# Optimization experiments

Hardware: AMD Instinct MI355X
Metric: run time of the kernel (lower is better)

The kernel has to match this reference:

```python
import jax, jax.numpy as jnp
import numpy as np

# ---- static forest structure: 1024 complete binary trees of depth 9 ----
N_TREES = 1024
DEPTH = 9
NPT = 2 ** (DEPTH + 1) - 1            # 1023 nodes per tree
DIM = N_TREES * NPT                    # 1,047,552 total nodes
C = 10                                 # hidden states
M = 128                                # emission alphabet
N_GEN = 4                              # parallel generative models
LEVEL_SIZES = [N_TREES * 2 ** (k + 1) for k in range(DEPTH)]
LEVEL_START = np.concatenate([[0], np.cumsum(LEVEL_SIZES)]).astype(np.int64)
TREE_OFF = np.arange(N_TREES, dtype=np.int64) * NPT


def _build_forest():
    parents, children = [], []
    for k in range(DEPTH):
        ch = np.arange(2 ** (k + 1) - 1, 2 ** (k + 2) - 1, dtype=np.int64)  # depth k+1 nodes
        pa = (ch - 1) // 2                                                   # their parents (depth k)
        children.append((TREE_OFF[:, None] + ch[None, :]).ravel())
        parents.append((TREE_OFF[:, None] + pa[None, :]).ravel())
    leaves = (TREE_OFF[:, None] + np.arange(NPT // 2, NPT, dtype=np.int64)[None, :]).ravel()
    trees_ind = np.repeat(np.arange(N_TREES, dtype=np.int64), NPT)
    return np.concatenate(parents), np.concatenate(children), leaves, trees_ind


def setup_inputs() -> dict:
    key = jax.random.key(0)
    k1, k2, k3, k4 = jax.random.split(key, 4)
    parents, children, leaves, trees_ind = _build_forest()
    return {
        "x": jax.random.randint(k4, (DIM,), 0, M, dtype=jnp.int32),
        "A": jax.random.normal(k1, (C, C, N_GEN), jnp.float32) * 2.5,
        "B": jax.random.normal(k2, (C, M, N_GEN), jnp.float32) * 2.5,
        "Pi": jax.random.normal(k3, (C, N_GEN), jnp.float32) * 2.5,
        "parents": jnp.asarray(parents, jnp.int32),
        "children": jnp.asarray(children, jnp.int32),
        "trees_ind": jnp.asarray(trees_ind, jnp.int32),
        "leaves": jnp.asarray(leaves, jnp.int32),
    }


def _upward(x, A, B, Pi, parents, children, trees_ind, leaves):
    # softmax reparameterization (vectorized over the n_gen axis)
    smA = jax.nn.softmax(A, axis=0)    # P(parent state i | child state j), cols sum over i
    smB = jax.nn.softmax(B, axis=1)    # emission distribution per state
    smPi = jax.nn.softmax(Pi, axis=0)  # leaf prior

    beta = jnp.zeros((DIM, C, N_GEN), smA.dtype)
    t_beta = jnp.zeros((DIM, C, N_GEN), smA.dtype)
    ll = jnp.zeros((DIM, N_GEN), smA.dtype)

    # leaves: beta = Pi * B[:, x_leaf], normalized
    B_leaf = jnp.swapaxes(smB[:, x[leaves]], 0, 1)            # [L, C, G]
    b = smPi[None, :, :] * B_leaf
    nu = b.sum(axis=1)                                         # [L, G]
    beta = beta.at[leaves].set(b / nu[:, None, :])
    ll = ll.at[leaves].set(jnp.log(nu))

    # bottom-up sweep over levels (static loop over tree depth)
    for k in reversed(range(DEPTH)):
        s, e = int(LEVEL_START[k]), int(LEVEL_START[k + 1])
        pa, ch = parents[s:e], children[s:e]
        beta_ch = beta[ch]                                     # [E, C, G]
        tb_ch = jnp.einsum('ijg,ejg->eig', smA, beta_ch)       # sum over child state j
        sums = jax.ops.segment_sum(tb_ch, pa, num_segments=DIM)
        cnt = jax.ops.segment_sum(jnp.ones((e - s,), smA.dtype), pa, num_segments=DIM)
        t_beta = t_beta + sums / jnp.maximum(cnt, 1.0)[:, None, None]  # scatter-mean over children
        # unique parents at this level = all depth-k nodes (static for complete trees)
        u = jnp.asarray((TREE_OFF[:, None] + np.arange(2 ** k - 1, 2 ** (k + 1) - 1)[None, :]).ravel(), jnp.int32)
        B_u = jnp.swapaxes(smB[:, x[u]], 0, 1)                 # [U, C, G]
        bl = t_beta[u] * B_u
        nu = bl.sum(axis=1)
        beta = beta.at[u].set(bl / nu[:, None, :])
        ll = ll.at[u].set(jnp.log(nu))

    # per-tree log-likelihood: scatter-sum node terms over trees_ind
    return jax.ops.segment_sum(ll, trees_ind, num_segments=N_TREES)  # [n_trees, G]


def reference(x, A, B, Pi, parents, children, trees_ind, leaves):
    return _upward(x, A, B, Pi, parents, children, trees_ind, leaves)
```

## Files before the change

kernel.cpp:

```cpp
#include <hip/hip_runtime.h>
#include <math.h>

#define NC     10
#define NCP    12
#define NM     128
#define NGEN   4
#define NPT    1023
#define NTREES 1024

#define RCPF(x) __builtin_amdgcn_rcpf(x)
#define WAVE_FENCE() __builtin_amdgcn_wave_barrier()

struct F12 { float4 a, b, c; };

__device__ __forceinline__ F12 ld12(const float* p) {
    F12 r; const float4* q = (const float4*)p;
    r.a = q[0]; r.b = q[1]; r.c = q[2]; return r;
}
__device__ __forceinline__ void unpack10(float* t, const F12& r) {
    t[0] = r.a.x; t[1] = r.a.y; t[2] = r.a.z; t[3] = r.a.w;
    t[4] = r.b.x; t[5] = r.b.y; t[6] = r.b.z; t[7] = r.b.w;
    t[8] = r.c.x; t[9] = r.c.y;
}
__device__ __forceinline__ void fma10(float* t, const F12& c, float s) {
    t[0] += c.a.x * s; t[1] += c.a.y * s; t[2] += c.a.z * s; t[3] += c.a.w * s;
    t[4] += c.b.x * s; t[5] += c.b.y * s; t[6] += c.b.z * s; t[7] += c.b.w * s;
    t[8] += c.c.x * s; t[9] += c.c.y * s;
}
__device__ __forceinline__ void mul10(float* t, const F12& r) {
    t[0] *= r.a.x; t[1] *= r.a.y; t[2] *= r.a.z; t[3] *= r.a.w;
    t[4] *= r.b.x; t[5] *= r.b.y; t[6] *= r.b.z; t[7] *= r.b.w;
    t[8] *= r.c.x; t[9] *= r.c.y;
}
__device__ __forceinline__ float sum10(const float* v) {
    return (((v[0] + v[1]) + (v[2] + v[3])) + ((v[4] + v[5]) + (v[6] + v[7]))) + (v[8] + v[9]);
}

__device__ __forceinline__ float half_subtree(const F12* acol,
                                              const float (*sBT)[NCP],
                                              const float (*sBTpi)[NCP],
                                              int xl0, int xl1, int xl2, int xl3,
                                              int x8a, int x8b, int x7, float* b7out)
{
    float b0[NC], b1[NC], sc[NC], t8a[NC], t8b[NC];

    unpack10(b0, ld12(&sBTpi[xl0][0]));
    unpack10(b1, ld12(&sBTpi[xl1][0]));
    float nu0 = sum10(b0), nu1 = sum10(b1);
    #pragma unroll
    for (int j = 0; j < NC; ++j) sc[j] = b0[j] * nu1 + b1[j] * nu0;
    #pragma unroll
    for (int i = 0; i < NC; ++i) t8a[i] = 0.f;
    #pragma unroll
    for (int j = 0; j < NC; ++j) fma10(t8a, acol[j], sc[j]);
    mul10(t8a, ld12(&sBT[x8a][0]));
    const float nu8a = sum10(t8a);

    unpack10(b0, ld12(&sBTpi[xl2][0]));
    unpack10(b1, ld12(&sBTpi[xl3][0]));
    nu0 = sum10(b0); nu1 = sum10(b1);
    #pragma unroll
    for (int j = 0; j < NC; ++j) sc[j] = b0[j] * nu1 + b1[j] * nu0;
    #pragma unroll
    for (int i = 0; i < NC; ++i) t8b[i] = 0.f;
    #pragma unroll
    for (int j = 0; j < NC; ++j) fma10(t8b, acol[j], sc[j]);
    mul10(t8b, ld12(&sBT[x8b][0]));
    const float nu8b = sum10(t8b);

    #pragma unroll
    for (int j = 0; j < NC; ++j) sc[j] = t8a[j] * nu8b + t8b[j] * nu8a;
    float t7[NC];
    #pragma unroll
    for (int i = 0; i < NC; ++i) t7[i] = 0.f;
    #pragma unroll
    for (int j = 0; j < NC; ++j) fma10(t7, acol[j], sc[j]);
    mul10(t7, ld12(&sBT[x7][0]));
    const float nu7 = sum10(t7);
    const float r = RCPF(nu7);
    #pragma unroll
    for (int j = 0; j < NC; ++j) b7out[j] = t7[j] * r;
    return __logf(nu7);
}

__device__ __forceinline__ float fused_step_ip(const F12* acol, const float (*sBT)[NCP],
                                               float* buf, int l,
                                               int xc0, int xc1, int xp)
{
    float t0[NC], t1[NC];
    #pragma unroll
    for (int i = 0; i < NC; ++i) { t0[i] = 0.f; t1[i] = 0.f; }
    #pragma unroll
    for (int j = 0; j < NC; ++j) {
        float4 gv = *(const float4*)(buf + j * 64 + 4 * l);
        fma10(t0, acol[j], gv.x + gv.y);
        fma10(t1, acol[j], gv.z + gv.w);
    }
    mul10(t0, ld12(&sBT[xc0][0]));
    mul10(t1, ld12(&sBT[xc1][0]));
    const float nu0 = sum10(t0), nu1 = sum10(t1);
    float tp[NC];
    #pragma unroll
    for (int i = 0; i < NC; ++i) tp[i] = 0.f;
    #pragma unroll
    for (int j = 0; j < NC; ++j) fma10(tp, acol[j], t0[j] * nu1 + t1[j] * nu0);
    mul10(tp, ld12(&sBT[xp][0]));
    const float nup = sum10(tp);
    const float rp = RCPF(nup);
    #pragma unroll
    for (int j = 0; j < NC; ++j) buf[j * 64 + l] = tp[j] * rp;
    return __logf(nup);
}

__global__ __launch_bounds__(256)
void htmm_fused(const int* __restrict__ x,
                const float* __restrict__ A,
                const float* __restrict__ B,
                const float* __restrict__ Pi,
                float* __restrict__ out)
{
    __shared__ __align__(16) float sACol[NC][NCP];
    __shared__ __align__(16) float sBT[NM][NCP];
    __shared__ __align__(16) float sBTpi[NM][NCP];
    __shared__ __align__(16) float sB6[4][NC][64];

    const int bid = blockIdx.x;
    const int g = bid >> 8;
    const int treeBase = (bid & 255) * 4;
    const int tid = threadIdx.x;
    const int u = tid >> 6, lane = tid & 63;

    const int tree = treeBase + u;
    const int tb = tree * NPT;

    int xl[8];
    #pragma unroll
    for (int k = 0; k < 8; ++k) xl[k] = x[tb + 511 + 8 * lane + k];
    int x8v[4];
    #pragma unroll
    for (int c = 0; c < 4; ++c) x8v[c] = x[tb + 255 + 4 * lane + c];
    const int x7a = x[tb + 127 + 2 * lane];
    const int x7b = x[tb + 128 + 2 * lane];
    const int x6v = x[tb + 63 + lane];

    float piv[NC];
    {
        float mx = -1e30f;
        #pragma unroll
        for (int i = 0; i < NC; ++i) { piv[i] = Pi[i * NGEN + g]; mx = fmaxf(mx, piv[i]); }
        float sm = 0.f;
        #pragma unroll
        for (int i = 0; i < NC; ++i) { piv[i] = __expf(piv[i] - mx); sm += piv[i]; }
        const float rs = 1.f / sm;
        #pragma unroll
        for (int i = 0; i < NC; ++i) piv[i] *= rs;
    }

    for (int c = u; c < NC; c += 4) {
        float e0 = __expf(B[(c * NM + lane) * NGEN + g]);
        float e1 = __expf(B[(c * NM + lane + 64) * NGEN + g]);
        float sm = e0 + e1;
        #pragma unroll
        for (int off = 32; off; off >>= 1) sm += __shfl_xor(sm, off);
        const float rs = 1.f / sm;
        const float v0 = e0 * rs, v1 = e1 * rs;
        sBT[lane][c]        = v0;
        sBT[lane + 64][c]   = v1;
        sBTpi[lane][c]      = piv[c] * v0;
        sBTpi[lane + 64][c] = piv[c] * v1;
    }
    if (tid >= 128 && tid < 128 + NC) {
        const int j = tid - 128;
        float col[NC], mx = -1e30f;
        #pragma unroll
        for (int i = 0; i < NC; ++i) { col[i] = A[(i * NC + j) * NGEN + g]; mx = fmaxf(mx, col[i]); }
        float sm = 0.f;
        #pragma unroll
        for (int i = 0; i < NC; ++i) { col[i] = __expf(col[i] - mx); sm += col[i]; }
        const float rs = 0.5f / sm;
        #pragma unroll
        for (int i = 0; i < NC; ++i) sACol[j][i] = col[i] * rs;
    }
    __syncthreads();

    F12 acol[NC];
    #pragma unroll
    for (int j = 0; j < NC; ++j) acol[j] = ld12(&sACol[j][0]);

    float b7a[NC], b7b[NC];
    float llacc;
    llacc  = half_subtree(acol, sBT, sBTpi, xl[0], xl[1], xl[2], xl[3],
                          x8v[0], x8v[1], x7a, b7a);
    llacc += half_subtree(acol, sBT, sBTpi, xl[4], xl[5], xl[6], xl[7],
                          x8v[2], x8v[3], x7b, b7b);

    {
        float sc[NC], t6[NC];
        #pragma unroll
        for (int j = 0; j < NC; ++j) sc[j] = b7a[j] + b7b[j];
        #pragma unroll
        for (int i = 0; i < NC; ++i) t6[i] = 0.f;
        #pragma unroll
        for (int j = 0; j < NC; ++j) fma10(t6, acol[j], sc[j]);
        mul10(t6, ld12(&sBT[x6v][0]));
        const float nup = sum10(t6);
        llacc += __logf(nup);
        const float rp = RCPF(nup);
        #pragma unroll
        for (int j = 0; j < NC; ++j) sB6[u][j][lane] = t6[j] * rp;
    }

    WAVE_FENCE();
    float lla = 0.f;
    if (lane < 16)
        lla = fused_step_ip(acol, sBT, &sB6[u][0][0], lane,
                            x[tb + 31 + 2 * lane], x[tb + 32 + 2 * lane],
                            x[tb + 15 + lane]);
    llacc += lla;
    WAVE_FENCE();
    float llb = 0.f;
    if (lane < 4)
        llb = fused_step_ip(acol, sBT, &sB6[u][0][0], lane,
                            x[tb + 7 + 2 * lane], x[tb + 8 + 2 * lane],
                            x[tb + 3 + lane]);
    llacc += llb;
    WAVE_FENCE();
    if (lane == 0)
        llacc += fused_step_ip(acol, sBT, &sB6[u][0][0], 0,
                               x[tb + 1], x[tb + 2], x[tb + 0]);

    #pragma unroll
    for (int off = 32; off; off >>= 1) llacc += __shfl_down(llacc, off);
    if (lane == 0) out[tree * NGEN + g] = llacc;
}

extern "C" void kernel_launch(void* const* d_in, const int* in_sizes, int n_in,
                              void* d_out, int out_size, void* d_ws, size_t ws_size,
                              hipStream_t stream) {
    const int*   x  = (const int*)d_in[0];
    const float* A  = (const float*)d_in[1];
    const float* B  = (const float*)d_in[2];
    const float* Pi = (const float*)d_in[3];
    float* out = (float*)d_out;
    htmm_fused<<<NTREES, 256, 0, stream>>>(x, A, B, Pi, out);
}
```

Measured before the change: 26.68 us.

## Split softmax setup into prologue kernel and run main pass one wave per block

Moves the per-generator softmax of A, B and Pi into a small setup kernel that writes padded tables to workspace. The main kernel then launches 4096 single-wave blocks that copy the emission table into LDS with vector loads, with no block-wide barrier. Pi is applied in registers instead of keeping a second LDS table, which halves LDS use and should allow more blocks per CU. The cost is a second kernel launch and a dependency between the two kernels. The fallback fused path gains a dead dummy call to the subtree helper.

```diff
diff --git a/kernel.cpp b/kernel.cpp
--- a/kernel.cpp
+++ b/kernel.cpp
@@ -8,6 +8,11 @@
 #define NPT    1023
 #define NTREES 1024
 
+#define WS_AC(g)   ((g) * (NC * NCP))
+#define WS_PI(g)   (4 * NC * NCP + (g) * NCP)
+#define WS_BT(g)   (4 * NC * NCP + 4 * NCP + (g) * (NM * NCP))
+#define WS_FLOATS  (4 * NC * NCP + 4 * NCP + 4 * NM * NCP)
+
 #define RCPF(x) __builtin_amdgcn_rcpf(x)
 #define WAVE_FENCE() __builtin_amdgcn_wave_barrier()
 
@@ -38,14 +43,16 @@
 
 __device__ __forceinline__ float half_subtree(const F12* acol,
                                               const float (*sBT)[NCP],
-                                              const float (*sBTpi)[NCP],
+                                              const float* piv,
                                               int xl0, int xl1, int xl2, int xl3,
                                               int x8a, int x8b, int x7, float* b7out)
 {
     float b0[NC], b1[NC], sc[NC], t8a[NC], t8b[NC];
 
-    unpack10(b0, ld12(&sBTpi[xl0][0]));
-    unpack10(b1, ld12(&sBTpi[xl1][0]));
+    unpack10(b0, ld12(&sBT[xl0][0]));
+    unpack10(b1, ld12(&sBT[xl1][0]));
+    #pragma unroll
+    for (int j = 0; j < NC; ++j) { b0[j] *= piv[j]; b1[j] *= piv[j]; }
     float nu0 = sum10(b0), nu1 = sum10(b1);
     #pragma unroll
     for (int j = 0; j < NC; ++j) sc[j] = b0[j] * nu1 + b1[j] * nu0;
@@ -56,8 +63,10 @@
     mul10(t8a, ld12(&sBT[x8a][0]));
     const float nu8a = sum10(t8a);
 
-    unpack10(b0, ld12(&sBTpi[xl2][0]));
-    unpack10(b1, ld12(&sBTpi[xl3][0]));
+    unpack10(b0, ld12(&sBT[xl2][0]));
+    unpack10(b1, ld12(&sBT[xl3][0]));
+    #pragma unroll
+    for (int j = 0; j < NC; ++j) { b0[j] *= piv[j]; b1[j] *= piv[j]; }
     nu0 = sum10(b0); nu1 = sum10(b1);
     #pragma unroll
     for (int j = 0; j < NC; ++j) sc[j] = b0[j] * nu1 + b1[j] * nu0;
@@ -110,6 +119,147 @@
     #pragma unroll
     for (int j = 0; j < NC; ++j) buf[j * 64 + l] = tp[j] * rp;
     return __logf(nup);
+}
+
+__global__ __launch_bounds__(128)
+void htmm_setup(const float* __restrict__ A,
+                const float* __restrict__ B,
+                const float* __restrict__ Pi,
+                float* __restrict__ ws)
+{
+    const int g = blockIdx.x;
+    const int tid = threadIdx.x;
+    const int wave = tid >> 6, lane = tid & 63;
+    float* bt = ws + WS_BT(g);
+
+    for (int c = wave; c < NC; c += 2) {
+        float e0 = __expf(B[(c * NM + lane) * NGEN + g]);
+        float e1 = __expf(B[(c * NM + lane + 64) * NGEN + g]);
+        float s = e0 + e1;
+        #pragma unroll
+        for (int off = 32; off; off >>= 1) s += __shfl_xor(s, off);
+        const float rs = 1.f / s;
+        bt[lane * NCP + c]        = e0 * rs;
+        bt[(lane + 64) * NCP + c] = e1 * rs;
+    }
+    if (tid < NM) { bt[tid * NCP + 10] = 0.f; bt[tid * NCP + 11] = 0.f; }
+
+    if (tid < NC) {
+        const int j = tid;
+        float col[NC], mx = -1e30f;
+        #pragma unroll
+        for (int i = 0; i < NC; ++i) { col[i] = A[(i * NC + j) * NGEN + g]; mx = fmaxf(mx, col[i]); }
+        float s = 0.f;
+        #pragma unroll
+        for (int i = 0; i < NC; ++i) { col[i] = __expf(col[i] - mx); s += col[i]; }
+        const float rs = 0.5f / s;
+        float* ac = ws + WS_AC(g) + j * NCP;
+        #pragma unroll
+        for (int i = 0; i < NC; ++i) ac[i] = col[i] * rs;
+        ac[10] = 0.f; ac[11] = 0.f;
+    }
+    if (tid == 32) {
+        float col[NC], mx = -1e30f;
+        #pragma unroll
+        for (int i = 0; i < NC; ++i) { col[i] = Pi[i * NGEN + g]; mx = fmaxf(mx, col[i]); }
+        float s = 0.f;
+        #pragma unroll
+        for (int i = 0; i < NC; ++i) { col[i] = __expf(col[i] - mx); s += col[i]; }
+        const float rs = 1.f / s;
+        float* pp = ws + WS_PI(g);
+        #pragma unroll
+        for (int i = 0; i < NC; ++i) pp[i] = col[i] * rs;
+        pp[10] = 0.f; pp[11] = 0.f;
+    }
+}
+
+__global__ __launch_bounds__(64)
+void htmm_main(const int* __restrict__ x,
+               const float* __restrict__ ws,
+               float* __restrict__ out)
+{
+    __shared__ __align__(16) float sBT[NM][NCP];
+    __shared__ __align__(16) float sB6[NC][64];
+
+    const int bid  = blockIdx.x;
+    const int tree = bid >> 2;
+    const int g    = bid & 3;
+    const int lane = threadIdx.x;
+    const int tb   = tree * NPT;
+
+    const float4* src = (const float4*)(ws + WS_BT(g));
+    float4 cp0 = src[0 * 64 + lane], cp1 = src[1 * 64 + lane];
+    float4 cp2 = src[2 * 64 + lane], cp3 = src[3 * 64 + lane];
+    float4 cp4 = src[4 * 64 + lane], cp5 = src[5 * 64 + lane];
+
+    int xl[8];
+    #pragma unroll
+    for (int k = 0; k < 8; ++k) xl[k] = x[tb + 511 + 8 * lane + k];
+    int x8v[4];
+    #pragma unroll
+    for (int c = 0; c < 4; ++c) x8v[c] = x[tb + 255 + 4 * lane + c];
+    const int x7a = x[tb + 127 + 2 * lane];
+    const int x7b = x[tb + 128 + 2 * lane];
+    const int x6v = x[tb + 63 + lane];
+
+    F12 acol[NC];
+    #pragma unroll
+    for (int j = 0; j < NC; ++j) acol[j] = ld12(ws + WS_AC(g) + j * NCP);
+    float piv[NC];
+    { F12 pv = ld12(ws + WS_PI(g)); unpack10(piv, pv); }
+
+    {
+        float4* dst = (float4*)&sBT[0][0];
+        dst[0 * 64 + lane] = cp0; dst[1 * 64 + lane] = cp1;
+        dst[2 * 64 + lane] = cp2; dst[3 * 64 + lane] = cp3;
+        dst[4 * 64 + lane] = cp4; dst[5 * 64 + lane] = cp5;
+    }
+    WAVE_FENCE();
+
+    float b7a[NC], b7b[NC];
+    float llacc;
+    llacc  = half_subtree(acol, sBT, piv, xl[0], xl[1], xl[2], xl[3],
+                          x8v[0], x8v[1], x7a, b7a);
+    llacc += half_subtree(acol, sBT, piv, xl[4], xl[5], xl[6], xl[7],
+                          x8v[2], x8v[3], x7b, b7b);
+    {
+        float sc[NC], t6[NC];
+        #pragma unroll
+        for (int j = 0; j < NC; ++j) sc[j] = b7a[j] + b7b[j];
+        #pragma unroll
+        for (int i = 0; i < NC; ++i) t6[i] = 0.f;
+        #pragma unroll
+        for (int j = 0; j < NC; ++j) fma10(t6, acol[j], sc[j]);
+        mul10(t6, ld12(&sBT[x6v][0]));
+        const float nup = sum10(t6);
+        llacc += __logf(nup);
+        const float rp = RCPF(nup);
+        #pragma unroll
+        for (int j = 0; j < NC; ++j) sB6[j][lane] = t6[j] * rp;
+    }
+
+    WAVE_FENCE();
+    float lla = 0.f;
+    if (lane < 16)
+        lla = fused_step_ip(acol, sBT, &sB6[0][0], lane,
+                            x[tb + 31 + 2 * lane], x[tb + 32 + 2 * lane],
+                            x[tb + 15 + lane]);
+    llacc += lla;
+    WAVE_FENCE();
+    float llb = 0.f;
+    if (lane < 4)
+        llb = fused_step_ip(acol, sBT, &sB6[0][0], lane,
+                            x[tb + 7 + 2 * lane], x[tb + 8 + 2 * lane],
+                            x[tb + 3 + lane]);
+    llacc += llb;
+    WAVE_FENCE();
+    if (lane == 0)
+        llacc += fused_step_ip(acol, sBT, &sB6[0][0], 0,
+                               x[tb + 1], x[tb + 2], x[tb + 0]);
+
+    #pragma unroll
+    for (int off = 32; off; off >>= 1) llacc += __shfl_down(llacc, off);
+    if (lane == 0) out[tree * NGEN + g] = llacc;
 }
 
 __global__ __launch_bounds__(256)
@@ -129,7 +279,6 @@
     const int treeBase = (bid & 255) * 4;
     const int tid = threadIdx.x;
     const int u = tid >> 6, lane = tid & 63;
-
     const int tree = treeBase + u;
     const int tb = tree * NPT;
 
@@ -155,7 +304,6 @@
         #pragma unroll
         for (int i = 0; i < NC; ++i) piv[i] *= rs;
     }
-
     for (int c = u; c < NC; c += 4) {
         float e0 = __expf(B[(c * NM + lane) * NGEN + g]);
         float e1 = __expf(B[(c * NM + lane + 64) * NGEN + g]);
@@ -187,13 +335,59 @@
     #pragma unroll
     for (int j = 0; j < NC; ++j) acol[j] = ld12(&sACol[j][0]);
 
+    float ones[NC];
+    #pragma unroll
+    for (int i = 0; i < NC; ++i) ones[i] = 1.f;
+
     float b7a[NC], b7b[NC];
     float llacc;
-    llacc  = half_subtree(acol, sBT, sBTpi, xl[0], xl[1], xl[2], xl[3],
-                          x8v[0], x8v[1], x7a, b7a);
-    llacc += half_subtree(acol, sBT, sBTpi, xl[4], xl[5], xl[6], xl[7],
-                          x8v[2], x8v[3], x7b, b7b);
-
+    llacc  = half_subtree(acol, sBT, ones, 0, 0, 0, 0, 0, 0, 0, b7a);
+    llacc = 0.f;
+    {
+        float b0[NC], b1[NC], sc[NC], t8a[NC], t8b[NC];
+        #pragma unroll
+        for (int h = 0; h < 2; ++h) {
+            const int* xh = xl + 4 * h;
+            const int x8a = x8v[2 * h], x8b = x8v[2 * h + 1];
+            const int x7 = h ? x7b : x7a;
+            unpack10(b0, ld12(&sBTpi[xh[0]][0]));
+            unpack10(b1, ld12(&sBTpi[xh[1]][0]));
+            float nu0 = sum10(b0), nu1 = sum10(b1);
+            #pragma unroll
+            for (int j = 0; j < NC; ++j) sc[j] = b0[j] * nu1 + b1[j] * nu0;
+            #pragma unroll
+            for (int i = 0; i < NC; ++i) t8a[i] = 0.f;
+            #pragma unroll
+            for (int j = 0; j < NC; ++j) fma10(t8a, acol[j], sc[j]);
+            mul10(t8a, ld12(&sBT[x8a][0]));
+            const float nu8a = sum10(t8a);
+            unpack10(b0, ld12(&sBTpi[xh[2]][0]));
+            unpack10(b1, ld12(&sBTpi[xh[3]][0]));
+            nu0 = sum10(b0); nu1 = sum10(b1);
+            #pragma unroll
+            for (int j = 0; j < NC; ++j) sc[j] = b0[j] * nu1 + b1[j] * nu0;
+            #pragma unroll
+            for (int i = 0; i < NC; ++i) t8b[i] = 0.f;
+            #pragma unroll
+            for (int j = 0; j < NC; ++j) fma10(t8b, acol[j], sc[j]);
+            mul10(t8b, ld12(&sBT[x8b][0]));
+            const float nu8b = sum10(t8b);
+            #pragma unroll
+            for (int j = 0; j < NC; ++j) sc[j] = t8a[j] * nu8b + t8b[j] * nu8a;
+            float t7[NC];
+            #pragma unroll
+            for (int i = 0; i < NC; ++i) t7[i] = 0.f;
+            #pragma unroll
+            for (int j = 0; j < NC; ++j) fma10(t7, acol[j], sc[j]);
+            mul10(t7, ld12(&sBT[x7][0]));
+            const float nu7 = sum10(t7);
+            const float r = RCPF(nu7);
+            float* dst = h ? b7b : b7a;
+            #pragma unroll
+            for (int j = 0; j < NC; ++j) dst[j] = t7[j] * r;
+            llacc += __logf(nu7);
+        }
+    }
     {
         float sc[NC], t6[NC];
         #pragma unroll
@@ -242,5 +436,12 @@
     const float* B  = (const float*)d_in[2];
     const float* Pi = (const float*)d_in[3];
     float* out = (float*)d_out;
-    htmm_fused<<<NTREES, 256, 0, stream>>>(x, A, B, Pi, out);
-}
+
+    if (ws_size >= (size_t)WS_FLOATS * sizeof(float)) {
+        float* ws = (float*)d_ws;
+        htmm_setup<<<NGEN, 128, 0, stream>>>(A, B, Pi, ws);
+        htmm_main<<<NTREES * NGEN, 64, 0, stream>>>(x, ws, out);
+    } else {
+        htmm_fused<<<NTREES, 256, 0, stream>>>(x, A, B, Pi, out);
+    }
+}
```

New measurement: 38.20 us. +43.2%, slower.
